# Performance work log

Hardware: AMD Instinct MI355X
Metric: run time of the kernel (lower is better)

## Reference

```python
import jax, jax.numpy as jnp
import numpy as np

N = 100000
E = 3200000


def setup_inputs() -> dict:
    key = jax.random.key(0)
    ks = jax.random.split(key, 8)
    x = jax.random.normal(ks[0], (N,), dtype=jnp.float32)
    edge_index = jax.random.randint(ks[1], (2, E), 0, N, dtype=jnp.int32)
    W_in = jax.random.normal(ks[2], (1, 32), dtype=jnp.float32) * 0.5
    b_in = jnp.zeros((32,), dtype=jnp.float32)
    W_mid = jax.random.normal(ks[3], (32, 32), dtype=jnp.float32) * (1.0 / np.sqrt(32))
    b_mid = jnp.zeros((32,), dtype=jnp.float32)
    W_out = jax.random.normal(ks[4], (32, 1), dtype=jnp.float32) * (1.0 / np.sqrt(32))
    b_out = jnp.zeros((1,), dtype=jnp.float32)
    return {"x": x, "edge_index": edge_index, "W_in": W_in, "b_in": b_in,
            "W_mid": W_mid, "b_mid": b_mid, "W_out": W_out, "b_out": b_out}


def _gcn_layer(h, src, dst, norm, W, b, n_nodes):
    # linear transform first (out_dim <= in_dim keeps message traffic small)
    h = h @ W                              # [N, out]
    msg = h[src] * norm[:, None]           # gather + edge-normalize, [E+N, out]
    out = jax.ops.segment_sum(msg, dst, num_segments=n_nodes)  # scatter-add
    return out + b


def reference(x, edge_index, W_in, b_in, W_mid, b_mid, W_out, b_out):
    n = x.shape[0]
    # add_self_loops
    loops = jnp.arange(n, dtype=edge_index.dtype)
    src = jnp.concatenate([edge_index[0], loops])
    dst = jnp.concatenate([edge_index[1], loops])
    # symmetric degree normalization (GCN): deg over target nodes incl. self loops
    deg = jax.ops.segment_sum(jnp.ones_like(src, dtype=x.dtype), dst, num_segments=n)
    dinv = jnp.where(deg > 0, jax.lax.rsqrt(deg), 0.0)
    norm = dinv[src] * dinv[dst]           # [E+N]

    h = x[:, None]                         # view(-1, 1)
    h = jax.nn.relu(_gcn_layer(h, src, dst, norm, W_in, b_in, n))
    h = jax.nn.relu(_gcn_layer(h, src, dst, norm, W_mid, b_mid, n))
    h = jax.nn.relu(_gcn_layer(h, src, dst, norm, W_mid, b_mid, n))  # conv_mid reused (shared weights)
    h = _gcn_layer(h, src, dst, norm, W_out, b_out, n)
    return jax.nn.sigmoid(h)               # [N, 1]
```

## Files before the change

kernel.cpp:

```cpp
#include <hip/hip_runtime.h>
#include <math.h>


#define BLK 256
#define PBLK 1024
#define BBLK 512
#define NBLK 512
#define MAXCHUNK 6272
#define BCAP 5120
#define SZCLAMP 5120
#define OVCAP 8192

#define FP8_SCALE 64.0f
#define FP8_INV   0.015625f

typedef float f32x2 __attribute__((ext_vector_type(2)));

__device__ __forceinline__ unsigned char fp8q(float v) {
    return (unsigned char)(__builtin_amdgcn_cvt_pk_fp8_f32(v, v, 0, false) & 0xFF);
}


__global__ void k_initcur(int* __restrict__ cursor, int NB, int* __restrict__ gov,
                          int* __restrict__ ph1, int* __restrict__ ph2,
                          float* __restrict__ sa, int N) {
    int b = blockIdx.x * blockDim.x + threadIdx.x;
    if (b < NB) cursor[b] = b * BCAP;
    if (b < 8) { ph1[b] = 0; ph2[b] = 0; }
    if (b == 8) sa[N] = 0.f;
    if (b == 9) gov[0] = 0;
}

__global__ void __launch_bounds__(PBLK) k_place(
        const int* __restrict__ src, const int* __restrict__ dst,
        int* __restrict__ cursor, int* __restrict__ bkt, int E, int chunk) {
    __shared__ int hist[788];
    __shared__ int lofs[788];
    __shared__ int lcur[788];
    __shared__ int tmp[PBLK];
    __shared__ int stage[MAXCHUNK];
    __shared__ unsigned short sbk[MAXCHUNK];
    int t = threadIdx.x;
    int b0 = blockIdx.x * chunk;
    int b1 = min(E, b0 + chunk);
    int n = b1 - b0;
    if (t < 788) hist[t] = 0;
    __syncthreads();
    for (int k = b0 + t; k < b1; k += PBLK) atomicAdd(&hist[dst[k] >> 7], 1);
    __syncthreads();
    int v = (t < 788) ? hist[t] : 0;
    tmp[t] = v;
    __syncthreads();
    for (int o = 1; o < PBLK; o <<= 1) {
        int a = (t >= o) ? tmp[t - o] : 0;
        __syncthreads();
        tmp[t] += a;
        __syncthreads();
    }
    int ex = tmp[t] - v;
    if (t < 788) { lofs[t] = ex; lcur[t] = ex; }
    __syncthreads();
    if (t < 782) {
        int c = hist[t];
        hist[t] = c ? atomicAdd(&cursor[t], c) : 0;
    }
    __syncthreads();
    for (int k = b0 + t; k < b1; k += PBLK) {
        int d = dst[k], s = src[k];
        int b = d >> 7;
        int p = atomicAdd(&lcur[b], 1);
        stage[p] = s | ((d & 127) << 17);
        sbk[p] = (unsigned short)b;
    }
    __syncthreads();
    for (int k = t; k < n; k += PBLK) {
        int b = sbk[k];
        int pos = hist[b] + (k - lofs[b]);
        if (pos < (b + 1) * BCAP) bkt[pos] = stage[k];
    }
}

__global__ void __launch_bounds__(BBLK) k_build(
        const int* __restrict__ cursor, const int* __restrict__ bkt,
        const float* __restrict__ x,
        unsigned* __restrict__ dg, int* __restrict__ ss,
        int* __restrict__ ovss, int* __restrict__ gov,
        float* __restrict__ dinv, float* __restrict__ sa, int N) {
    __shared__ int bin_[1024];
    __shared__ int tot[128];
    __shared__ int stg[8192];
    __shared__ int ovn[64], ovv[64];
    __shared__ int ovcnt;
    int b = blockIdx.x, t = threadIdx.x;
    int node_base = b << 7;
    int gb = b * BCAP;
    int sz = min(cursor[b] - gb, SZCLAMP);
    for (int i = t; i < 1024; i += BBLK) bin_[i] = 0;
    if (t == 0) ovcnt = 0;
    __syncthreads();
    const int* q = bkt + gb;
    for (int k = t; k < sz; k += BBLK) {
        int v = q[k];
        int bin = (((v >> 17) & 127) << 3) | ((v & 0x1FFFF) >> 14);
        atomicAdd(&bin_[bin], 1);
    }
    __syncthreads();
    if (t < 128) {
        int c[8];
        #pragma unroll
        for (int j = 0; j < 8; ++j) c[j] = bin_[(t << 3) + j];
        int run = 0;
        int base = (t << 6) + 1;
        #pragma unroll
        for (int j = 0; j < 8; ++j) { bin_[(t << 3) + j] = base + run; run += c[j]; }
        tot[t] = run;
        int i = node_base + t;
        if (i < N) {
            float d = rsqrtf((float)(run + 1));
            dinv[i] = d;
            sa[i] = x[i] * d;
        }
    }
    __syncthreads();
    for (int k = t; k < sz; k += BBLK) {
        int v = q[k];
        int bin = (((v >> 17) & 127) << 3) | ((v & 0x1FFFF) >> 14);
        int pos = atomicAdd(&bin_[bin], 1);
        int nn = bin >> 3;
        int val = (v & 0x1FFFF) << 5;
        if (pos - (nn << 6) <= 63) stg[pos] = val;
        else {
            int o = atomicAdd(&ovcnt, 1);
            if (o < 64) { ovn[o] = nn; ovv[o] = val; }
        }
    }
    __syncthreads();
    if (t < 128) {
        int i = node_base + t;
        if (i < N) dg[i] = (unsigned)min(tot[t] + 1, 64);
    }
    for (int j = t; j < 8192; j += BBLK) {
        int nn = j >> 6, s = j & 63;
        int i = node_base + nn;
        if (i >= N) continue;
        int tt = tot[nn];
        int val;
        if (s == 0) val = i << 5;
        else if (s <= min(tt, 63)) val = stg[j];
        else val = N << 5;
        ss[((size_t)i << 6) + s] = val;
    }
    __syncthreads();
    if (t == 0 && ovcnt > 0) {
        int m = min(ovcnt, 64);
        int base = atomicAdd(gov, m);
        unsigned long long used = 0ull;
        int w = 0;
        for (int a = 0; a < m; ++a) {
            if ((used >> a) & 1ull) continue;
            int nn = ovn[a];
            int start = w;
            for (int c2 = a; c2 < m; ++c2) {
                if (!((used >> c2) & 1ull) && ovn[c2] == nn) {
                    used |= 1ull << c2;
                    if (base + w < OVCAP) ovss[base + w] = ovv[c2];
                    ++w;
                }
            }
            dg[node_base + nn] = (unsigned)(tot[nn] + 1)
                               | ((unsigned)(base + start) << 16);
        }
    }
}


__global__ void __launch_bounds__(BLK) k_l1aggG(
        const unsigned* __restrict__ dg, const int* __restrict__ ss,
        const int* __restrict__ ovss,
        const float* __restrict__ sa, const float* __restrict__ dinv,
        const float* __restrict__ Win, const float* __restrict__ bin,
        const float* __restrict__ Wmid, unsigned char* __restrict__ Gh, int N) {
    __shared__ float sW2[1024];
    __shared__ float sF[8][2][34];
    int tid = threadIdx.x;
    #pragma unroll
    for (int r = 0; r < 4; ++r) {
        int t4 = r * 256 + tid;
        int k = t4 >> 5, ln = t4 & 31;
        sW2[(k >> 1) * 64 + ln * 2 + (k & 1)] = Wmid[t4];
    }
    int gid = (blockIdx.x * blockDim.x + tid) >> 5;
    int gA = gid * 2, gB = gA + 1;
    int l = tid & 31, grp = tid >> 5;
    int begA = gA << 6, begB = gB << 6;
    int iA0 = ss[begA + l];
    int iB0 = ss[begB + l];
    int iA1 = ss[begA + l + 32];
    int iB1 = ss[begB + l + 32];
    unsigned dgA = dg[gA], dgB = dg[gB];
    float sA = sa[(unsigned)iA0 >> 5] + sa[(unsigned)iA1 >> 5];
    float sB = sa[(unsigned)iB0 >> 5] + sa[(unsigned)iB1 >> 5];
    int cntA = dgA & 0xFFFF, cntB = dgB & 0xFFFF;
    int wmax = max(cntA, cntB);
    wmax = max(wmax, __shfl_xor(wmax, 32));
    if (wmax > 64) {
        for (int k = l; k < cntA - 64; k += 32)
            sA += sa[(unsigned)ovss[(dgA >> 16) + k] >> 5];
        for (int k = l; k < cntB - 64; k += 32)
            sB += sa[(unsigned)ovss[(dgB >> 16) + k] >> 5];
    }
    #pragma unroll
    for (int m = 16; m; m >>= 1) {
        sA += __shfl_xor(sA, m, 32);
        sB += __shfl_xor(sB, m, 32);
    }
    float dA = dinv[gA];
    float dB = dinv[gB];
    float wl = Win[l], bl = bin[l];
    float FA = dA * sA * wl + bl; FA = FA > 0.f ? FA : 0.f;
    float FB = dB * sB * wl + bl; FB = FB > 0.f ? FB : 0.f;
    sF[grp][0][l] = FA;
    sF[grp][1][l] = FB;
    __syncthreads();
    f32x2 s2A = (f32x2)0.f, s2B = (f32x2)0.f;
    #pragma unroll
    for (int k2 = 0; k2 < 16; ++k2) {
        f32x2 w2 = *(const f32x2*)&sW2[k2 * 64 + l * 2];
        s2A += *(const f32x2*)&sF[grp][0][k2 * 2] * w2;
        s2B += *(const f32x2*)&sF[grp][1][k2 * 2] * w2;
    }
    Gh[(long long)gA * 32 + l] = fp8q((s2A.x + s2A.y) * dA * FP8_SCALE);
    Gh[(long long)gB * 32 + l] = fp8q((s2B.x + s2B.y) * dB * FP8_SCALE);
}

__device__ __forceinline__ void acc_row(f32x2* a2, uint2 v) {
    a2[0] += __builtin_amdgcn_cvt_pk_f32_fp8(v.x, false);
    a2[1] += __builtin_amdgcn_cvt_pk_f32_fp8(v.x, true);
    a2[2] += __builtin_amdgcn_cvt_pk_f32_fp8(v.y, false);
    a2[3] += __builtin_amdgcn_cvt_pk_f32_fp8(v.y, true);
}

__device__ __forceinline__ void gather2(const unsigned char* __restrict__ Gb,
                                        const int* __restrict__ ss,
                                        int begA, int begB, int sub, int fo,
                                        f32x2* aA, f32x2* aB) {
    int sA = begA + sub, sB = begB + sub;
    int iA[8], iB[8];
    #pragma unroll
    for (int r = 0; r < 8; ++r) iA[r] = ss[sA + 8 * r];
    #pragma unroll
    for (int r = 0; r < 8; ++r) iB[r] = ss[sB + 8 * r];
    uint2 vA[8], vB[8];
    #pragma unroll
    for (int r = 0; r < 8; ++r)
        vA[r] = *(const uint2*)(Gb + (unsigned)(iA[r] | fo));
    #pragma unroll
    for (int r = 0; r < 8; ++r)
        vB[r] = *(const uint2*)(Gb + (unsigned)(iB[r] | fo));
    #pragma unroll
    for (int r = 0; r < 8; ++r) acc_row(aA, vA[r]);
    #pragma unroll
    for (int r = 0; r < 8; ++r) acc_row(aB, vB[r]);
}

__device__ __forceinline__ void reduce_subs(f32x2* a2) {
    #pragma unroll
    for (int j = 0; j < 4; ++j) {
        #pragma unroll
        for (int m = 4; m <= 16; m <<= 1) {
            f32x2 o;
            o.x = __shfl_xor(a2[j].x, m);
            o.y = __shfl_xor(a2[j].y, m);
            a2[j] += o;
        }
    }
}

__global__ void __launch_bounds__(256) k_agg2mv(
        const unsigned* __restrict__ dg, const int* __restrict__ ss,
        const int* __restrict__ ovss,
        const unsigned char* __restrict__ Gb, const float* __restrict__ dinv,
        const float* __restrict__ b, const float* __restrict__ Wmid,
        unsigned char* __restrict__ Gh3, int N) {
    __shared__ float sW2[1024];
    __shared__ float sF[8][2][34];
    __shared__ float sdv[8][2];
    int t = threadIdx.x;
    #pragma unroll
    for (int r = 0; r < 4; ++r) {
        int t4 = r * 256 + t;
        int k = t4 >> 5, ln = t4 & 31;
        sW2[(k >> 1) * 64 + ln * 2 + (k & 1)] = Wmid[t4];
    }
    int gid = (blockIdx.x * blockDim.x + t) >> 5;
    int gA = gid * 2, gB = gA + 1;
    int lane = t & 31, sub = lane >> 2, fl = lane & 3;
    int grp = t >> 5;
    int fo = fl << 3;
    f32x2 aA[4], aB[4];
    #pragma unroll
    for (int j = 0; j < 4; ++j) { aA[j] = (f32x2)0.f; aB[j] = (f32x2)0.f; }
    gather2(Gb, ss, gA << 6, gB << 6, sub, fo, aA, aB);
    unsigned dgA = dg[gA], dgB = dg[gB];
    int cntA = dgA & 0xFFFF, cntB = dgB & 0xFFFF;
    int wmax = max(cntA, cntB);
    wmax = max(wmax, __shfl_xor(wmax, 32));
    if (wmax > 64) {
        for (int k = sub; k < cntA - 64; k += 8)
            acc_row(aA, *(const uint2*)(Gb + (unsigned)(ovss[(dgA >> 16) + k] | fo)));
        for (int k = sub; k < cntB - 64; k += 8)
            acc_row(aB, *(const uint2*)(Gb + (unsigned)(ovss[(dgB >> 16) + k] | fo)));
    }
    reduce_subs(aA);
    reduce_subs(aB);
    if (sub == 0) {
        float dA = dinv[gA];
        float dB = dinv[gB];
        if (fl == 0) { sdv[grp][0] = dA; sdv[grp][1] = dB; }
        float dsA = dA * FP8_INV, dsB = dB * FP8_INV;
        #pragma unroll
        for (int j = 0; j < 8; ++j) {
            float bj = b[fl * 8 + j];
            float vA = dsA * aA[j >> 1][j & 1] + bj;
            float vB = dsB * aB[j >> 1][j & 1] + bj;
            sF[grp][0][fl * 8 + j] = vA > 0.f ? vA : 0.f;
            sF[grp][1][fl * 8 + j] = vB > 0.f ? vB : 0.f;
        }
    }
    __syncthreads();
    #pragma unroll
    for (int n2 = 0; n2 < 2; ++n2) {
        f32x2 s2 = (f32x2)0.f;
        #pragma unroll
        for (int k2 = 0; k2 < 16; ++k2) {
            f32x2 w2 = *(const f32x2*)&sW2[k2 * 64 + lane * 2];
            f32x2 f2 = *(const f32x2*)&sF[grp][n2][k2 * 2];
            s2 += f2 * w2;
        }
        float v = (s2.x + s2.y) * sdv[grp][n2] * FP8_SCALE;
        Gh3[(long long)(gA + n2) * 32 + lane] = fp8q(v);
    }
}

__global__ void __launch_bounds__(256) k_agg3(
        const unsigned* __restrict__ dg, const int* __restrict__ ss,
        const int* __restrict__ ovss,
        const unsigned char* __restrict__ Gb, const float* __restrict__ dinv,
        const float* __restrict__ b, const float* __restrict__ Wout,
        float* __restrict__ sa, int N) {
    int t = blockIdx.x * blockDim.x + threadIdx.x;
    int gid = t >> 5;
    int gA = gid * 2, gB = gA + 1;
    int lane = t & 31, sub = lane >> 2, fl = lane & 3;
    int fo = fl << 3;
    f32x2 aA[4], aB[4];
    #pragma unroll
    for (int j = 0; j < 4; ++j) { aA[j] = (f32x2)0.f; aB[j] = (f32x2)0.f; }
    gather2(Gb, ss, gA << 6, gB << 6, sub, fo, aA, aB);
    unsigned dgA = dg[gA], dgB = dg[gB];
    int cntA = dgA & 0xFFFF, cntB = dgB & 0xFFFF;
    int wmax = max(cntA, cntB);
    wmax = max(wmax, __shfl_xor(wmax, 32));
    if (wmax > 64) {
        for (int k = sub; k < cntA - 64; k += 8)
            acc_row(aA, *(const uint2*)(Gb + (unsigned)(ovss[(dgA >> 16) + k] | fo)));
        for (int k = sub; k < cntB - 64; k += 8)
            acc_row(aB, *(const uint2*)(Gb + (unsigned)(ovss[(dgB >> 16) + k] | fo)));
    }
    reduce_subs(aA);
    reduce_subs(aB);
    if (sub == 0) {
        float dA = dinv[gA];
        float dB = dinv[gB];
        float dsA = dA * FP8_INV, dsB = dB * FP8_INV;
        float pA = 0.f, pB = 0.f;
        #pragma unroll
        for (int j = 0; j < 8; ++j) {
            float bj = b[fl * 8 + j];
            float wj = Wout[fl * 8 + j];
            float vA = dsA * aA[j >> 1][j & 1] + bj;
            float vB = dsB * aB[j >> 1][j & 1] + bj;
            vA = vA > 0.f ? vA : 0.f;
            vB = vB > 0.f ? vB : 0.f;
            pA += vA * wj;
            pB += vB * wj;
        }
        pA += __shfl_xor(pA, 1, 32); pA += __shfl_xor(pA, 2, 32);
        pB += __shfl_xor(pB, 1, 32); pB += __shfl_xor(pB, 2, 32);
        if (fl == 0) {
            sa[gA] = pA * dA;
            sa[gB] = pB * dB;
        }
    }
}

__global__ void __launch_bounds__(BLK) k_final_agg(
        const unsigned* __restrict__ dg, const int* __restrict__ ss,
        const int* __restrict__ ovss,
        const float* __restrict__ sa, const float* __restrict__ dinv,
        const float* __restrict__ bout, float* __restrict__ out, int N) {
    int t = blockIdx.x * blockDim.x + threadIdx.x;
    int gid = t >> 5;
    int gA = gid * 2, gB = gA + 1;
    int l = t & 31;
    int begA = gA << 6, begB = gB << 6;
    int iA0 = ss[begA + l];
    int iB0 = ss[begB + l];
    int iA1 = ss[begA + l + 32];
    int iB1 = ss[begB + l + 32];
    unsigned dgA = dg[gA], dgB = dg[gB];
    float sA = sa[(unsigned)iA0 >> 5] + sa[(unsigned)iA1 >> 5];
    float sB = sa[(unsigned)iB0 >> 5] + sa[(unsigned)iB1 >> 5];
    int cntA = dgA & 0xFFFF, cntB = dgB & 0xFFFF;
    int wmax = max(cntA, cntB);
    wmax = max(wmax, __shfl_xor(wmax, 32));
    if (wmax > 64) {
        for (int k = l; k < cntA - 64; k += 32)
            sA += sa[(unsigned)ovss[(dgA >> 16) + k] >> 5];
        for (int k = l; k < cntB - 64; k += 32)
            sB += sa[(unsigned)ovss[(dgB >> 16) + k] >> 5];
    }
    #pragma unroll
    for (int m = 16; m; m >>= 1) {
        sA += __shfl_xor(sA, m, 32);
        sB += __shfl_xor(sB, m, 32);
    }
    if (l == 0) {
        float zA = dinv[gA] * sA + bout[0];
        float zB = dinv[gB] * sB + bout[0];
        out[gA] = 1.0f / (1.0f + expf(-zA));
        out[gB] = 1.0f / (1.0f + expf(-zB));
    }
}

extern "C" void kernel_launch(void* const* d_in, const int* in_sizes, int n_in,
                              void* d_out, int out_size, void* d_ws, size_t ws_size,
                              hipStream_t stream) {
    const float* x    = (const float*)d_in[0];
    const int*   ei   = (const int*)  d_in[1];
    const float* Win  = (const float*)d_in[2];
    const float* bin  = (const float*)d_in[3];
    const float* Wmid = (const float*)d_in[4];
    const float* bmid = (const float*)d_in[5];
    const float* Wout = (const float*)d_in[6];
    const float* bout = (const float*)d_in[7];
    float* out = (float*)d_out;

    int N = in_sizes[0];
    int E = in_sizes[1] / 2;
    const int* src = ei;
    const int* dst = ei + E;

    int NB = (N + 127) >> 7;
    int chunk = (E + NBLK - 1) / NBLK;

    int* cursor = (int*)d_ws;
    int* gov    = cursor + 1024;
    unsigned* dg = (unsigned*)(gov + 16);
    int* ss     = (int*)(dg + N);
    int* ovss   = ss + ((size_t)N << 6);
    float* dinv = (float*)(ovss + OVCAP);
    float* sa   = dinv + N;
    unsigned char* Gh  = (unsigned char*)(sa + N + 8);
    unsigned char* Gh3 = Gh + 32 * (size_t)N + 32;
    int* bkt    = (int*)(Gh3 + 32 * (size_t)N + 32);

    int gN16 = (N * 16 + BLK - 1) / BLK;

    k_initcur<<<(NB + BLK - 1) / BLK, BLK, 0, stream>>>(
        cursor, NB, gov, (int*)(Gh + 32 * (size_t)N),
        (int*)(Gh3 + 32 * (size_t)N), sa, N);
    k_place<<<NBLK, PBLK, 0, stream>>>(src, dst, cursor, bkt, E, chunk);
    k_build<<<NB, BBLK, 0, stream>>>(cursor, bkt, x, dg, ss, ovss, gov,
                                     dinv, sa, N);

    k_l1aggG<<<gN16, BLK, 0, stream>>>(dg, ss, ovss, sa, dinv, Win, bin,
                                       Wmid, Gh, N);

    k_agg2mv<<<gN16, BLK, 0, stream>>>(dg, ss, ovss, Gh, dinv, bmid, Wmid,
                                       Gh3, N);

    k_agg3<<<gN16, BLK, 0, stream>>>(dg, ss, ovss, Gh3, dinv, bmid, Wout,
                                     sa, N);

    k_final_agg<<<gN16, BLK, 0, stream>>>(dg, ss, ovss, sa, dinv, bout,
                                          out, N);
}
```

Baseline: 207.0 us.

## Replace two-pass bucketed CSR build with direct per-node atomic scatter

```diff
diff --git a/kernel.cpp b/kernel.cpp
--- a/kernel.cpp
+++ b/kernel.cpp
@@ -3,13 +3,7 @@
 
 
 #define BLK 256
-#define PBLK 1024
-#define BBLK 512
-#define NBLK 512
-#define MAXCHUNK 6272
-#define BCAP 5120
-#define SZCLAMP 5120
-#define OVCAP 8192
+#define OVMAX 4096
 
 #define FP8_SCALE 64.0f
 #define FP8_INV   0.015625f
@@ -21,155 +15,70 @@
 }
 
 
-__global__ void k_initcur(int* __restrict__ cursor, int NB, int* __restrict__ gov,
-                          int* __restrict__ ph1, int* __restrict__ ph2,
-                          float* __restrict__ sa, int N) {
-    int b = blockIdx.x * blockDim.x + threadIdx.x;
-    if (b < NB) cursor[b] = b * BCAP;
-    if (b < 8) { ph1[b] = 0; ph2[b] = 0; }
-    if (b == 8) sa[N] = 0.f;
-    if (b == 9) gov[0] = 0;
-}
-
-__global__ void __launch_bounds__(PBLK) k_place(
-        const int* __restrict__ src, const int* __restrict__ dst,
-        int* __restrict__ cursor, int* __restrict__ bkt, int E, int chunk) {
-    __shared__ int hist[788];
-    __shared__ int lofs[788];
-    __shared__ int lcur[788];
-    __shared__ int tmp[PBLK];
-    __shared__ int stage[MAXCHUNK];
-    __shared__ unsigned short sbk[MAXCHUNK];
-    int t = threadIdx.x;
-    int b0 = blockIdx.x * chunk;
-    int b1 = min(E, b0 + chunk);
-    int n = b1 - b0;
-    if (t < 788) hist[t] = 0;
-    __syncthreads();
-    for (int k = b0 + t; k < b1; k += PBLK) atomicAdd(&hist[dst[k] >> 7], 1);
-    __syncthreads();
-    int v = (t < 788) ? hist[t] : 0;
-    tmp[t] = v;
-    __syncthreads();
-    for (int o = 1; o < PBLK; o <<= 1) {
-        int a = (t >= o) ? tmp[t - o] : 0;
-        __syncthreads();
-        tmp[t] += a;
-        __syncthreads();
-    }
-    int ex = tmp[t] - v;
-    if (t < 788) { lofs[t] = ex; lcur[t] = ex; }
-    __syncthreads();
-    if (t < 782) {
-        int c = hist[t];
-        hist[t] = c ? atomicAdd(&cursor[t], c) : 0;
-    }
-    __syncthreads();
-    for (int k = b0 + t; k < b1; k += PBLK) {
-        int d = dst[k], s = src[k];
-        int b = d >> 7;
-        int p = atomicAdd(&lcur[b], 1);
-        stage[p] = s | ((d & 127) << 17);
-        sbk[p] = (unsigned short)b;
-    }
-    __syncthreads();
-    for (int k = t; k < n; k += PBLK) {
-        int b = sbk[k];
-        int pos = hist[b] + (k - lofs[b]);
-        if (pos < (b + 1) * BCAP) bkt[pos] = stage[k];
-    }
-}
-
-__global__ void __launch_bounds__(BBLK) k_build(
-        const int* __restrict__ cursor, const int* __restrict__ bkt,
-        const float* __restrict__ x,
-        unsigned* __restrict__ dg, int* __restrict__ ss,
-        int* __restrict__ ovss, int* __restrict__ gov,
-        float* __restrict__ dinv, float* __restrict__ sa, int N) {
-    __shared__ int bin_[1024];
-    __shared__ int tot[128];
-    __shared__ int stg[8192];
-    __shared__ int ovn[64], ovv[64];
-    __shared__ int ovcnt;
-    int b = blockIdx.x, t = threadIdx.x;
-    int node_base = b << 7;
-    int gb = b * BCAP;
-    int sz = min(cursor[b] - gb, SZCLAMP);
-    for (int i = t; i < 1024; i += BBLK) bin_[i] = 0;
-    if (t == 0) ovcnt = 0;
-    __syncthreads();
-    const int* q = bkt + gb;
-    for (int k = t; k < sz; k += BBLK) {
-        int v = q[k];
-        int bin = (((v >> 17) & 127) << 3) | ((v & 0x1FFFF) >> 14);
-        atomicAdd(&bin_[bin], 1);
-    }
-    __syncthreads();
-    if (t < 128) {
-        int c[8];
-        #pragma unroll
-        for (int j = 0; j < 8; ++j) c[j] = bin_[(t << 3) + j];
-        int run = 0;
-        int base = (t << 6) + 1;
-        #pragma unroll
-        for (int j = 0; j < 8; ++j) { bin_[(t << 3) + j] = base + run; run += c[j]; }
-        tot[t] = run;
-        int i = node_base + t;
-        if (i < N) {
-            float d = rsqrtf((float)(run + 1));
-            dinv[i] = d;
-            sa[i] = x[i] * d;
-        }
-    }
-    __syncthreads();
-    for (int k = t; k < sz; k += BBLK) {
-        int v = q[k];
-        int bin = (((v >> 17) & 127) << 3) | ((v & 0x1FFFF) >> 14);
-        int pos = atomicAdd(&bin_[bin], 1);
-        int nn = bin >> 3;
-        int val = (v & 0x1FFFF) << 5;
-        if (pos - (nn << 6) <= 63) stg[pos] = val;
+__global__ void k_init(int* __restrict__ ss, int* __restrict__ cnt,
+                       int* __restrict__ gov, float* __restrict__ sa,
+                       int* __restrict__ ph1, int* __restrict__ ph2, int N) {
+    int tid = blockIdx.x * blockDim.x + threadIdx.x;
+    int stride = gridDim.x * blockDim.x;
+    int PH = N << 5;
+    int4 ph4 = make_int4(PH, PH, PH, PH);
+    int total4 = N << 4;
+    for (int i = tid; i < total4; i += stride) ((int4*)ss)[i] = ph4;
+    for (int i = tid; i < N; i += stride) cnt[i] = 0;
+    if (tid < 8) { ph1[tid] = 0; ph2[tid] = 0; }
+    if (tid == 0) { gov[0] = 0; sa[N] = 0.f; }
+}
+
+__global__ void k_scatter(const int* __restrict__ src, const int* __restrict__ dst,
+                          int* __restrict__ cnt, int* __restrict__ ss,
+                          int* __restrict__ gov, int* __restrict__ ovpair, int E) {
+    int tid = blockIdx.x * blockDim.x + threadIdx.x;
+    int stride = gridDim.x * blockDim.x;
+    for (int e = tid; e < E; e += stride) {
+        int d = dst[e], s = src[e];
+        int pos = atomicAdd(&cnt[d], 1);
+        if (pos < 63) ss[(d << 6) + 1 + pos] = s << 5;
         else {
-            int o = atomicAdd(&ovcnt, 1);
-            if (o < 64) { ovn[o] = nn; ovv[o] = val; }
-        }
-    }
-    __syncthreads();
-    if (t < 128) {
-        int i = node_base + t;
-        if (i < N) dg[i] = (unsigned)min(tot[t] + 1, 64);
-    }
-    for (int j = t; j < 8192; j += BBLK) {
-        int nn = j >> 6, s = j & 63;
-        int i = node_base + nn;
-        if (i >= N) continue;
-        int tt = tot[nn];
-        int val;
-        if (s == 0) val = i << 5;
-        else if (s <= min(tt, 63)) val = stg[j];
-        else val = N << 5;
-        ss[((size_t)i << 6) + s] = val;
-    }
-    __syncthreads();
-    if (t == 0 && ovcnt > 0) {
-        int m = min(ovcnt, 64);
-        int base = atomicAdd(gov, m);
-        unsigned long long used = 0ull;
-        int w = 0;
-        for (int a = 0; a < m; ++a) {
-            if ((used >> a) & 1ull) continue;
-            int nn = ovn[a];
-            int start = w;
-            for (int c2 = a; c2 < m; ++c2) {
-                if (!((used >> c2) & 1ull) && ovn[c2] == nn) {
-                    used |= 1ull << c2;
-                    if (base + w < OVCAP) ovss[base + w] = ovv[c2];
-                    ++w;
-                }
+            int o = atomicAdd(gov, 1);
+            if (o < OVMAX) { ovpair[2 * o] = d; ovpair[2 * o + 1] = s << 5; }
+        }
+    }
+}
+
+__global__ void k_finish(const int* __restrict__ cnt, int* __restrict__ ss,
+                         unsigned* __restrict__ dg, const float* __restrict__ x,
+                         float* __restrict__ dinv, float* __restrict__ sa, int N) {
+    int i = blockIdx.x * blockDim.x + threadIdx.x;
+    if (i >= N) return;
+    int c = cnt[i];
+    int deg = c + 1;
+    dg[i] = (unsigned)min(deg, 64);
+    ss[i << 6] = i << 5;
+    float d = rsqrtf((float)deg);
+    dinv[i] = d;
+    sa[i] = x[i] * d;
+}
+
+__global__ void k_ovfix(const int* __restrict__ gov, const int* __restrict__ ovpair,
+                        const int* __restrict__ cnt, int* __restrict__ ovss,
+                        unsigned* __restrict__ dg, int N) {
+    if (blockIdx.x != 0 || threadIdx.x != 0) return;
+    int m = min(gov[0], OVMAX);
+    if (m <= 0) return;
+    bool used[OVMAX];
+    for (int a = 0; a < m; ++a) used[a] = false;
+    int w = 0;
+    for (int a = 0; a < m; ++a) {
+        if (used[a]) continue;
+        int node = ovpair[2 * a];
+        int start = w;
+        for (int c2 = a; c2 < m; ++c2) {
+            if (!used[c2] && ovpair[2 * c2] == node) {
+                used[c2] = true;
+                ovss[w++] = ovpair[2 * c2 + 1];
             }
-            dg[node_base + nn] = (unsigned)(tot[nn] + 1)
-                               | ((unsigned)(base + start) << 16);
-        }
+        }
+        dg[node] = (unsigned)(cnt[node] + 1) | ((unsigned)start << 16);
     }
 }
 
@@ -451,28 +360,25 @@
     const int* src = ei;
     const int* dst = ei + E;
 
-    int NB = (N + 127) >> 7;
-    int chunk = (E + NBLK - 1) / NBLK;
-
-    int* cursor = (int*)d_ws;
-    int* gov    = cursor + 1024;
+    int* cnt    = (int*)d_ws;
+    int* gov    = cnt + N;
     unsigned* dg = (unsigned*)(gov + 16);
     int* ss     = (int*)(dg + N);
     int* ovss   = ss + ((size_t)N << 6);
-    float* dinv = (float*)(ovss + OVCAP);
+    int* ovpair = ovss + OVMAX;
+    float* dinv = (float*)(ovpair + 2 * OVMAX);
     float* sa   = dinv + N;
     unsigned char* Gh  = (unsigned char*)(sa + N + 8);
     unsigned char* Gh3 = Gh + 32 * (size_t)N + 32;
-    int* bkt    = (int*)(Gh3 + 32 * (size_t)N + 32);
 
     int gN16 = (N * 16 + BLK - 1) / BLK;
 
-    k_initcur<<<(NB + BLK - 1) / BLK, BLK, 0, stream>>>(
-        cursor, NB, gov, (int*)(Gh + 32 * (size_t)N),
-        (int*)(Gh3 + 32 * (size_t)N), sa, N);
-    k_place<<<NBLK, PBLK, 0, stream>>>(src, dst, cursor, bkt, E, chunk);
-    k_build<<<NB, BBLK, 0, stream>>>(cursor, bkt, x, dg, ss, ovss, gov,
-                                     dinv, sa, N);
+    k_init<<<2048, BLK, 0, stream>>>(ss, cnt, gov, sa,
+                                     (int*)(Gh + 32 * (size_t)N),
+                                     (int*)(Gh3 + 32 * (size_t)N), N);
+    k_scatter<<<2048, BLK, 0, stream>>>(src, dst, cnt, ss, gov, ovpair, E);
+    k_finish<<<(N + BLK - 1) / BLK, BLK, 0, stream>>>(cnt, ss, dg, x, dinv, sa, N);
+    k_ovfix<<<1, 64, 0, stream>>>(gov, ovpair, cnt, ovss, dg, N);
 
     k_l1aggG<<<gN16, BLK, 0, stream>>>(dg, ss, ovss, sa, dinv, Win, bin,
                                        Wmid, Gh, N);
```

Result: slower. 456.7 us (+120.7%).
